# Kernel optimization log

Hardware: AMD Instinct MI355X
Metric: run time of the kernel (lower is better)

Reference implementation:

```python
import jax, jax.numpy as jnp
import numpy as np

B, N, D = 4, 4096, 1024


def setup_inputs() -> dict:
    key = jax.random.key(0)
    ks = jax.random.split(key, 7)
    s = 1.0 / np.sqrt(D)
    return {
        "x": jax.random.normal(ks[0], (B, N, D), dtype=jnp.float32),
        "Wq": jax.random.uniform(ks[1], (D, D), jnp.float32, -s, s),
        "bq": jax.random.uniform(ks[2], (D,), jnp.float32, -s, s),
        "Wk": jax.random.uniform(ks[3], (D, D), jnp.float32, -s, s),
        "bk": jax.random.uniform(ks[4], (D,), jnp.float32, -s, s),
        "Wv": jax.random.uniform(ks[5], (D, D), jnp.float32, -s, s),
        "bv": jax.random.uniform(ks[6], (D,), jnp.float32, -s, s),
    }


def reference(x, Wq, bq, Wk, bk, Wv, bv):
    # Projections (nn.Linear: x @ W.T + b; here W stored as [in, out])
    Q = x @ Wq + bq
    K = x @ Wk + bk
    V = x @ Wv + bv
    Qp = jax.nn.elu(Q) + 1.0  # positive feature map
    Kp = jax.nn.elu(K) + 1.0
    KV = jnp.einsum('bnd,bne->bde', Kp, V)          # [B, D, D]
    numerator = jnp.einsum('bnd,bde->bne', Qp, KV)  # [B, N, D]
    K_sum = Kp.sum(axis=1)                           # [B, D]
    norm = jnp.einsum('bnd,bd->bn', Qp, K_sum)[..., None]
    eps = 1e-6
    return numerator / (norm + eps)
```

## Files before the change

kernel.cpp:

```cpp
#include <hip/hip_runtime.h>
#include <hip/hip_bf16.h>
#include <cstdint>

typedef __bf16 bf16x8 __attribute__((ext_vector_type(8)));
typedef float  f32x4  __attribute__((ext_vector_type(4)));
typedef unsigned short u16x8 __attribute__((ext_vector_type(8)));

__device__ __forceinline__ unsigned short f2bf(float f) {
  __hip_bfloat16 h = __float2bfloat16(f);
  return __builtin_bit_cast(unsigned short, h);
}
__device__ __forceinline__ float bf2f(unsigned short u) {
  return __builtin_bit_cast(float, (unsigned)u << 16);
}

#define GL2LDS16(gp, lp)                                                      \
  __builtin_amdgcn_global_load_lds(                                           \
      (const __attribute__((address_space(1))) unsigned int*)(gp),            \
      (__attribute__((address_space(3))) unsigned int*)(lp), 16, 0, 0)

#define SBAR                                                                  \
  {                                                                           \
    __builtin_amdgcn_s_barrier();                                             \
    __builtin_amdgcn_sched_barrier(0);                                        \
  }
#define WAITV(n)                                                              \
  {                                                                           \
    asm volatile("s_waitcnt vmcnt(" #n ")" ::: "memory");                     \
    __builtin_amdgcn_sched_barrier(0);                                        \
  }
#define WAITL0                                                                \
  {                                                                           \
    asm volatile("s_waitcnt lgkmcnt(0)" ::: "memory");                        \
    __builtin_amdgcn_sched_barrier(0);                                        \
  }

template <int MODE>
__global__ __launch_bounds__(512, 2) void gemm256(
    const unsigned short* __restrict__ A, long long lda, long long aOffZ,
    const unsigned short* __restrict__ B, long long ldb, long long bOffZ,
    void* __restrict__ C, long long ldc, long long cOffZ,
    const float* __restrict__ bias, const float* __restrict__ bias2,
    const float* __restrict__ norm, long long normOffZ,
    float* __restrict__ ksum, int K) {
  __shared__ __attribute__((aligned(16))) char lds[4 * 32768];
  const int t = threadIdx.x;
  const int wave = t >> 6, lane = t & 63;
  const int wm = wave >> 2, wn = wave & 3;
  const int fr = lane & 15, fq = lane >> 4;

  const int gx = gridDim.x, gy = gridDim.y;
  int flat = blockIdx.y * gx + blockIdx.x;
  const int total = gx * gy;
  if ((total & 7) == 0) flat = (flat & 7) * (total >> 3) + (flat >> 3);
  int bx, by;
  if (MODE == 1) {
    bx = flat / gy;
    by = flat - bx * gy;
  } else {
    bx = flat % gx;
    by = flat / gx;
  }
  const int m0 = by * 256, n0 = bx * 256;

  const long long z = blockIdx.z;
  long long aBase, bBase;
  if (MODE == 3) {
    const long long koff = (z & 3) * 4096 + (z >> 2) * 1024;
    aBase = koff;
    bBase = koff;
  } else {
    aBase = z * aOffZ;
    bBase = z * bOffZ;
  }
  const unsigned short* Az = A + aBase;
  const unsigned short* Bz = B + bBase;

  const unsigned short* gA[2];
  const unsigned short* gB[2];
#pragma unroll
  for (int c = 0; c < 2; ++c) {
    int d = c * 8192 + t * 16;
    int l = d ^ (((d >> 7) & 3) << 4);
    int row = l >> 6, kel = (l & 63) >> 1;
    gA[c] = Az + (long long)(m0 + row) * lda + kel;
    gB[c] = Bz + (long long)(n0 + row) * ldb + kel;
  }

  const int slotx = (fr >> 1) & 3;
  const int abase = wm * 8192 + fr * 64 + ((fq ^ slotx) << 4);
  const int bbase = 16384 + wn * 4096 + fr * 64 + ((fq ^ slotx) << 4);

  f32x4 acc[8][4];
#pragma unroll
  for (int i = 0; i < 8; ++i)
#pragma unroll
    for (int j = 0; j < 4; ++j) acc[i][j] = (f32x4){0.f, 0.f, 0.f, 0.f};

  const int NT = K >> 5;

  auto stage = [&](int tile) {
    const int k0 = tile << 5;
    char* bufp = lds + (tile & 3) * 32768;
#pragma unroll
    for (int c = 0; c < 2; ++c)
      GL2LDS16(gA[c] + k0, bufp + c * 8192 + wave * 1024);
#pragma unroll
    for (int c = 0; c < 2; ++c)
      GL2LDS16(gB[c] + k0, bufp + 16384 + c * 8192 + wave * 1024);
  };

  stage(0);
  stage(1);
  stage(2);
  WAITV(8);
  SBAR;

  bf16x8 av[8], bv[4];
  for (int tt = 0; tt < NT - 3; ++tt) {
    const char* bufp = lds + (tt & 3) * 32768;
#pragma unroll
    for (int i = 0; i < 4; ++i) {
      av[i] = *(const bf16x8*)(bufp + abase + i * 1024);
      av[4 + i] = *(const bf16x8*)(bufp + abase + 4096 + i * 1024);
      bv[i] = *(const bf16x8*)(bufp + bbase + i * 1024);
    }
    stage(tt + 3);
    SBAR;
    WAITL0;
    __builtin_amdgcn_s_setprio(1);
#pragma unroll
    for (int mi = 0; mi < 8; ++mi)
#pragma unroll
      for (int ni = 0; ni < 4; ++ni)
        acc[mi][ni] = __builtin_amdgcn_mfma_f32_16x16x32_bf16(
            av[mi], bv[ni], acc[mi][ni], 0, 0, 0);
    __builtin_amdgcn_s_setprio(0);
    WAITV(8);
    SBAR;
  }

  WAITV(0);
  SBAR;
#pragma unroll
  for (int e = 0; e < 3; ++e) {
    const char* bufp = lds + ((NT - 3 + e) & 3) * 32768;
#pragma unroll
    for (int i = 0; i < 4; ++i) {
      av[i] = *(const bf16x8*)(bufp + abase + i * 1024);
      av[4 + i] = *(const bf16x8*)(bufp + abase + 4096 + i * 1024);
      bv[i] = *(const bf16x8*)(bufp + bbase + i * 1024);
    }
#pragma unroll
    for (int mi = 0; mi < 8; ++mi)
#pragma unroll
      for (int ni = 0; ni < 4; ++ni)
        acc[mi][ni] = __builtin_amdgcn_mfma_f32_16x16x32_bf16(
            av[mi], bv[ni], acc[mi][ni], 0, 0, 0);
  }

  const float* nrmz = (MODE == 4) ? (norm + z * normOffZ) : nullptr;
  float* Cf = (float*)C + z * cOffZ;
  unsigned short* Cu = (unsigned short*)C + z * cOffZ;
  const bool lower = (m0 < 1024);
  const int bidx = n0 >> 12;
#pragma unroll
  for (int mi = 0; mi < 8; ++mi) {
    const int rbase = m0 + wm * 128 + mi * 16 + fq * 4;
    float rb[4], nv[4], ks[4];
#pragma unroll
    for (int j = 0; j < 4; ++j) {
      if (MODE == 1)
        rb[j] = lower ? bias[rbase + j] : bias2[rbase - 1024 + j];
      if (MODE == 4) nv[j] = nrmz[rbase + j];
      ks[j] = 0.f;
    }
#pragma unroll
    for (int ni = 0; ni < 4; ++ni) {
      const int c = n0 + wn * 64 + ni * 16 + fr;
      float cb = 0.f;
      if (MODE == 0) cb = bias[c];
#pragma unroll
      for (int j = 0; j < 4; ++j) {
        float v = acc[mi][ni][j];
        if (MODE == 0) v += cb;
        if (MODE == 1) v += rb[j];
        if (MODE == 0 || (MODE == 1 && lower))
          v = (v > 0.f) ? v + 1.f : __expf(v);
        if (MODE == 1 && lower) ks[j] += v;
        const long long ci = (long long)(rbase + j) * ldc + c;
        if (MODE == 4)
          Cf[ci] = v / nv[j];
        else
          Cu[ci] = f2bf(v);
      }
    }
    if (MODE == 1 && lower) {
#pragma unroll
      for (int j = 0; j < 4; ++j) {
        float s = ks[j];
        s += __shfl_xor(s, 1, 16);
        s += __shfl_xor(s, 2, 16);
        s += __shfl_xor(s, 4, 16);
        s += __shfl_xor(s, 8, 16);
        if (fr == 0) atomicAdd(&ksum[bidx * 1024 + rbase + j], s);
      }
    }
  }
}

__global__ __launch_bounds__(256) void reduce_kvt(
    const unsigned short* __restrict__ P, unsigned short* __restrict__ KVt) {
  const long long i = ((long long)blockIdx.x * 256 + threadIdx.x) * 8;
  const int b = (int)(i >> 20);
  const long long ed = i & ((1ll << 20) - 1);
  float s[8] = {0.f, 0.f, 0.f, 0.f, 0.f, 0.f, 0.f, 0.f};
#pragma unroll
  for (int ks = 0; ks < 4; ++ks) {
    u16x8 v = *(const u16x8*)(P + ((long long)(ks * 4 + b) << 20) + ed);
#pragma unroll
    for (int j = 0; j < 8; ++j) s[j] += bf2f(v[j]);
  }
  u16x8 o;
#pragma unroll
  for (int j = 0; j < 8; ++j) o[j] = f2bf(s[j]);
  *(u16x8*)(KVt + i) = o;
}

__global__ __launch_bounds__(256) void transpose_w(
    const float* __restrict__ W, unsigned short* __restrict__ WT) {
  __shared__ float tile[32][33];
  const int tx = threadIdx.x & 31, ty = threadIdx.x >> 5;
  const int i0 = blockIdx.y * 32, o0 = blockIdx.x * 32;
#pragma unroll
  for (int s = 0; s < 32; s += 8)
    tile[ty + s][tx] = W[(long long)(i0 + ty + s) * 1024 + o0 + tx];
  __syncthreads();
#pragma unroll
  for (int s = 0; s < 32; s += 8)
    WT[(long long)(o0 + ty + s) * 1024 + i0 + tx] = f2bf(tile[tx][ty + s]);
}

__global__ __launch_bounds__(256) void convert_x(
    const float4* __restrict__ in, uint2* __restrict__ out, int n4) {
  const int stride = gridDim.x * blockDim.x;
  for (int i = blockIdx.x * blockDim.x + threadIdx.x; i < n4; i += stride) {
    float4 v = in[i];
    uint2 o;
    o.x = (unsigned)f2bf(v.x) | ((unsigned)f2bf(v.y) << 16);
    o.y = (unsigned)f2bf(v.z) | ((unsigned)f2bf(v.w) << 16);
    out[i] = o;
  }
}

__global__ __launch_bounds__(256) void norm_kernel(
    const unsigned short* __restrict__ Qp, const float* __restrict__ Ksum,
    float* __restrict__ nrm) {
  const int gw = (blockIdx.x * 256 + threadIdx.x) >> 6;
  const int lane = threadIdx.x & 63;
  const int b = gw >> 12;
  const unsigned short* q = Qp + (long long)gw * 1024;
  const float* ks = Ksum + b * 1024;
  float s = 0.f;
  for (int i = lane; i < 1024; i += 64) s += bf2f(q[i]) * ks[i];
#pragma unroll
  for (int o = 32; o > 0; o >>= 1) s += __shfl_down(s, o, 64);
  if (lane == 0) nrm[gw] = s + 1e-6f;
}

extern "C" void kernel_launch(void* const* d_in, const int* in_sizes, int n_in,
                              void* d_out, int out_size, void* d_ws,
                              size_t ws_size, hipStream_t stream) {
  const float* x  = (const float*)d_in[0];
  const float* Wq = (const float*)d_in[1];
  const float* bq = (const float*)d_in[2];
  const float* Wk = (const float*)d_in[3];
  const float* bk = (const float*)d_in[4];
  const float* Wv = (const float*)d_in[5];
  const float* bv = (const float*)d_in[6];
  float* out = (float*)d_out;

  const size_t MN = 16384ull * 1024ull;
  char* w = (char*)d_ws;
  unsigned short* xb  = (unsigned short*)w;  w += MN * 2;
  unsigned short* WT  = (unsigned short*)w;  w += 3ull * 1024 * 1024 * 2;
  unsigned short* Qp  = (unsigned short*)w;  w += MN * 2;
  unsigned short* KVb = (unsigned short*)w;  w += 2 * MN * 2;
  unsigned short* KVt = (unsigned short*)w;  w += 4ull * 1024 * 1024 * 2;
  float* Ksum = (float*)w;  w += 4ull * 1024 * 4;
  float* nrm  = (float*)w;  w += 16384ull * 4;
  unsigned short* Pkv = xb;
  unsigned short* KpT = KVb;
  unsigned short* VT  = KVb + MN;

  hipMemsetAsync(Ksum, 0, 4096 * sizeof(float), stream);
  transpose_w<<<dim3(32, 32), 256, 0, stream>>>(Wq, WT);
  transpose_w<<<dim3(32, 32), 256, 0, stream>>>(Wk, WT + 1024 * 1024);
  transpose_w<<<dim3(32, 32), 256, 0, stream>>>(Wv, WT + 2 * 1024 * 1024);
  convert_x<<<2048, 256, 0, stream>>>((const float4*)x, (uint2*)xb,
                                      (int)(MN / 4));

  gemm256<0><<<dim3(4, 64, 1), 512, 0, stream>>>(
      xb, 1024, 0, WT, 1024, 0, Qp, 1024, 0, bq, nullptr, nullptr, 0, nullptr,
      1024);
  gemm256<1><<<dim3(64, 8, 1), 512, 0, stream>>>(
      WT + 1024 * 1024, 1024, 0, xb, 1024, 0, KVb, 16384, 0, bk, bv, nullptr,
      0, Ksum, 1024);
  gemm256<3><<<dim3(4, 4, 16), 512, 0, stream>>>(
      VT, 16384, 0, KpT, 16384, 0, Pkv, 1024, 1024 * 1024, nullptr, nullptr,
      nullptr, 0, nullptr, 1024);
  reduce_kvt<<<2048, 256, 0, stream>>>(Pkv, KVt);
  norm_kernel<<<4096, 256, 0, stream>>>(Qp, Ksum, nrm);
  gemm256<4><<<dim3(4, 16, 4), 512, 0, stream>>>(
      Qp, 1024, 4096ll * 1024, KVt, 1024, 1024 * 1024, out, 1024,
      4096ll * 1024, nullptr, nullptr, nrm, 4096, nullptr, 1024);
}
```

Before: 271.6 us.

## Drop mid-loop GEMM barrier, move Ksum to separate kernel, vectorize norm

The GEMM main loop now issues the next global-to-LDS stage before its LDS fragment reads and drops the extra barrier between them. It relies on the end-of-iteration barrier to guarantee the target buffer is no longer being read. The K-sum is no longer accumulated with shuffles and atomics in the MODE 1 epilogue. A new ksum_kernel instead reduces KpT, which removes the memset and the atomics but adds a re-read of a 32MB intermediate. norm_kernel now uses 16-byte vector loads instead of scalar strided loads.

```diff
diff --git a/kernel.cpp b/kernel.cpp
--- a/kernel.cpp
+++ b/kernel.cpp
@@ -41,8 +41,7 @@
     const unsigned short* __restrict__ B, long long ldb, long long bOffZ,
     void* __restrict__ C, long long ldc, long long cOffZ,
     const float* __restrict__ bias, const float* __restrict__ bias2,
-    const float* __restrict__ norm, long long normOffZ,
-    float* __restrict__ ksum, int K) {
+    const float* __restrict__ norm, long long normOffZ, int K) {
   __shared__ __attribute__((aligned(16))) char lds[4 * 32768];
   const int t = threadIdx.x;
   const int wave = t >> 6, lane = t & 63;
@@ -119,14 +118,13 @@
   bf16x8 av[8], bv[4];
   for (int tt = 0; tt < NT - 3; ++tt) {
     const char* bufp = lds + (tt & 3) * 32768;
+    stage(tt + 3);
 #pragma unroll
     for (int i = 0; i < 4; ++i) {
       av[i] = *(const bf16x8*)(bufp + abase + i * 1024);
       av[4 + i] = *(const bf16x8*)(bufp + abase + 4096 + i * 1024);
       bv[i] = *(const bf16x8*)(bufp + bbase + i * 1024);
     }
-    stage(tt + 3);
-    SBAR;
     WAITL0;
     __builtin_amdgcn_s_setprio(1);
 #pragma unroll
@@ -163,17 +161,15 @@
   float* Cf = (float*)C + z * cOffZ;
   unsigned short* Cu = (unsigned short*)C + z * cOffZ;
   const bool lower = (m0 < 1024);
-  const int bidx = n0 >> 12;
 #pragma unroll
   for (int mi = 0; mi < 8; ++mi) {
     const int rbase = m0 + wm * 128 + mi * 16 + fq * 4;
-    float rb[4], nv[4], ks[4];
+    float rb[4], nv[4];
 #pragma unroll
     for (int j = 0; j < 4; ++j) {
       if (MODE == 1)
         rb[j] = lower ? bias[rbase + j] : bias2[rbase - 1024 + j];
       if (MODE == 4) nv[j] = nrmz[rbase + j];
-      ks[j] = 0.f;
     }
 #pragma unroll
     for (int ni = 0; ni < 4; ++ni) {
@@ -187,23 +183,11 @@
         if (MODE == 1) v += rb[j];
         if (MODE == 0 || (MODE == 1 && lower))
           v = (v > 0.f) ? v + 1.f : __expf(v);
-        if (MODE == 1 && lower) ks[j] += v;
         const long long ci = (long long)(rbase + j) * ldc + c;
         if (MODE == 4)
           Cf[ci] = v / nv[j];
         else
           Cu[ci] = f2bf(v);
-      }
-    }
-    if (MODE == 1 && lower) {
-#pragma unroll
-      for (int j = 0; j < 4; ++j) {
-        float s = ks[j];
-        s += __shfl_xor(s, 1, 16);
-        s += __shfl_xor(s, 2, 16);
-        s += __shfl_xor(s, 4, 16);
-        s += __shfl_xor(s, 8, 16);
-        if (fr == 0) atomicAdd(&ksum[bidx * 1024 + rbase + j], s);
       }
     }
   }
@@ -253,16 +237,42 @@
   }
 }
 
+__global__ __launch_bounds__(256) void ksum_kernel(
+    const unsigned short* __restrict__ KpT, float* __restrict__ Ksum) {
+  const int gw = (blockIdx.x * 256 + threadIdx.x) >> 6;
+  const int lane = threadIdx.x & 63;
+  const int d = gw >> 2, b = gw & 3;
+  const unsigned short* p = KpT + (long long)d * 16384 + b * 4096 + lane * 8;
+  float s = 0.f;
+#pragma unroll
+  for (int it = 0; it < 8; ++it) {
+    u16x8 v = *(const u16x8*)(p + it * 512);
+#pragma unroll
+    for (int j = 0; j < 8; ++j) s += bf2f(v[j]);
+  }
+#pragma unroll
+  for (int o = 32; o > 0; o >>= 1) s += __shfl_down(s, o, 64);
+  if (lane == 0) Ksum[b * 1024 + d] = s;
+}
+
 __global__ __launch_bounds__(256) void norm_kernel(
     const unsigned short* __restrict__ Qp, const float* __restrict__ Ksum,
     float* __restrict__ nrm) {
   const int gw = (blockIdx.x * 256 + threadIdx.x) >> 6;
   const int lane = threadIdx.x & 63;
   const int b = gw >> 12;
-  const unsigned short* q = Qp + (long long)gw * 1024;
-  const float* ks = Ksum + b * 1024;
+  const unsigned short* q = Qp + (long long)gw * 1024 + lane * 8;
+  const float* ks = Ksum + b * 1024 + lane * 8;
   float s = 0.f;
-  for (int i = lane; i < 1024; i += 64) s += bf2f(q[i]) * ks[i];
+#pragma unroll
+  for (int it = 0; it < 2; ++it) {
+    u16x8 v = *(const u16x8*)(q + it * 512);
+    float4 k0 = *(const float4*)(ks + it * 512);
+    float4 k1 = *(const float4*)(ks + it * 512 + 4);
+    s += bf2f(v[0]) * k0.x + bf2f(v[1]) * k0.y + bf2f(v[2]) * k0.z +
+         bf2f(v[3]) * k0.w + bf2f(v[4]) * k1.x + bf2f(v[5]) * k1.y +
+         bf2f(v[6]) * k1.z + bf2f(v[7]) * k1.w;
+  }
 #pragma unroll
   for (int o = 32; o > 0; o >>= 1) s += __shfl_down(s, o, 64);
   if (lane == 0) nrm[gw] = s + 1e-6f;
@@ -293,7 +303,6 @@
   unsigned short* KpT = KVb;
   unsigned short* VT  = KVb + MN;
 
-  hipMemsetAsync(Ksum, 0, 4096 * sizeof(float), stream);
   transpose_w<<<dim3(32, 32), 256, 0, stream>>>(Wq, WT);
   transpose_w<<<dim3(32, 32), 256, 0, stream>>>(Wk, WT + 1024 * 1024);
   transpose_w<<<dim3(32, 32), 256, 0, stream>>>(Wv, WT + 2 * 1024 * 1024);
@@ -301,17 +310,17 @@
                                       (int)(MN / 4));
 
   gemm256<0><<<dim3(4, 64, 1), 512, 0, stream>>>(
-      xb, 1024, 0, WT, 1024, 0, Qp, 1024, 0, bq, nullptr, nullptr, 0, nullptr,
-      1024);
+      xb, 1024, 0, WT, 1024, 0, Qp, 1024, 0, bq, nullptr, nullptr, 0, 1024);
   gemm256<1><<<dim3(64, 8, 1), 512, 0, stream>>>(
       WT + 1024 * 1024, 1024, 0, xb, 1024, 0, KVb, 16384, 0, bk, bv, nullptr,
-      0, Ksum, 1024);
+      0, 1024);
+  ksum_kernel<<<1024, 256, 0, stream>>>(KpT, Ksum);
   gemm256<3><<<dim3(4, 4, 16), 512, 0, stream>>>(
       VT, 16384, 0, KpT, 16384, 0, Pkv, 1024, 1024 * 1024, nullptr, nullptr,
-      nullptr, 0, nullptr, 1024);
+      nullptr, 0, 1024);
   reduce_kvt<<<2048, 256, 0, stream>>>(Pkv, KVt);
   norm_kernel<<<4096, 256, 0, stream>>>(Qp, Ksum, nrm);
   gemm256<4><<<dim3(4, 16, 4), 512, 0, stream>>>(
       Qp, 1024, 4096ll * 1024, KVt, 1024, 1024 * 1024, out, 1024,
-      4096ll * 1024, nullptr, nullptr, nrm, 4096, nullptr, 1024);
-}
+      4096ll * 1024, nullptr, nullptr, nrm, 4096, 1024);
+}
```

New measurement: 254.8 us. -6.2%, faster.
